# Kernel optimization log

Measured on AMD Instinct MI355X. Metric: run time of the kernel, lower is better.

## Reference

```python
import jax, jax.numpy as jnp
import numpy as np
from jax import lax

B, K, C = 8, 65536, 128
NUM_PROPOSAL = 1024


def furthest_point_sample(xyz, n):
    """xyz: (B,K,3) -> (B,n) int32 indices, matching pointnet2 FPS."""
    b, k, _ = xyz.shape
    init_far = jnp.zeros((b,), dtype=jnp.int32)          # first picked point = index 0
    init_dist = jnp.full((b, k), 1e10, dtype=xyz.dtype)  # running min squared distance

    def step(carry, _):
        dist, far = carry
        pt = jnp.take_along_axis(xyz, far[:, None, None].astype(jnp.int32), axis=1)  # (B,1,3)
        d = jnp.sum((xyz - pt) ** 2, axis=-1)            # (B,K)
        dist = jnp.minimum(dist, d)
        far = jnp.argmax(dist, axis=-1).astype(jnp.int32)
        return (dist, far), far

    (_, _), rest = lax.scan(step, (init_dist, init_far), None, length=n - 1)  # rest: (n-1,B)
    inds = jnp.concatenate([init_far[None, :], rest], axis=0)                  # (n,B)
    return jnp.transpose(inds, (1, 0))                                         # (B,n)


def setup_inputs() -> dict:
    key = jax.random.key(0)
    k1, k2 = jax.random.split(key)
    xyz = jax.random.normal(k1, (B, K, 3), dtype=jnp.float32)
    features = jax.random.normal(k2, (B, C, K), dtype=jnp.float32)
    return {"xyz": xyz, "features": features}


def reference(xyz, features):
    sample_inds = furthest_point_sample(xyz, NUM_PROPOSAL)            # (B,n)
    # gather_operation(xyz^T, inds)^T -> (B,n,3)
    new_xyz = jnp.take_along_axis(xyz, sample_inds[:, :, None], axis=1)
    # gather_operation(features, inds) -> (B,C,n)
    new_features = jnp.take_along_axis(features, sample_inds[:, None, :], axis=2)
    return (new_xyz, new_features, sample_inds)
```

## Files before the change

kernel.cpp:

```cpp
#include <hip/hip_runtime.h>
#include <stdint.h>

#define BATCH 8
#define K 65536
#define CFEAT 128
#define NPROP 1024
#define M 16
#define T 320
#define CTHREADS 256
#define PTS (K / M)
#define PPT (PTS / CTHREADS)

#define OUT_FEAT (BATCH * NPROP * 3)
#define OUT_INDS (BATCH * NPROP * 3 + BATCH * CFEAT * NPROP)

#define SLOT_STRIDE 8
#define WS_ULLS (2 * BATCH * M * SLOT_STRIDE)

__global__ __launch_bounds__(256) void fps_init(unsigned long long* ws) {
    int i = blockIdx.x * 256 + threadIdx.x;
    if (i < WS_ULLS) ws[i] = 0ull;
}

__device__ __forceinline__ unsigned int wave_umax63(unsigned int x) {
    int v = (int)x;
    int t;
    t = __builtin_amdgcn_update_dpp(v, v, 0x111, 0xF, 0xF, false);
    v = ((unsigned)t > (unsigned)v) ? t : v;
    t = __builtin_amdgcn_update_dpp(v, v, 0x112, 0xF, 0xF, false);
    v = ((unsigned)t > (unsigned)v) ? t : v;
    t = __builtin_amdgcn_update_dpp(v, v, 0x114, 0xF, 0xF, false);
    v = ((unsigned)t > (unsigned)v) ? t : v;
    t = __builtin_amdgcn_update_dpp(v, v, 0x118, 0xF, 0xF, false);
    v = ((unsigned)t > (unsigned)v) ? t : v;
    t = __builtin_amdgcn_update_dpp(v, v, 0x142, 0xF, 0xF, false);
    v = ((unsigned)t > (unsigned)v) ? t : v;
    t = __builtin_amdgcn_update_dpp(v, v, 0x143, 0xF, 0xF, false);
    v = ((unsigned)t > (unsigned)v) ? t : v;
    return (unsigned int)v;
}

__device__ __forceinline__ unsigned int row16_umax15(unsigned int x) {
    int v = (int)x;
    int t;
    t = __builtin_amdgcn_update_dpp(v, v, 0x111, 0xF, 0xF, false);
    v = ((unsigned)t > (unsigned)v) ? t : v;
    t = __builtin_amdgcn_update_dpp(v, v, 0x112, 0xF, 0xF, false);
    v = ((unsigned)t > (unsigned)v) ? t : v;
    t = __builtin_amdgcn_update_dpp(v, v, 0x114, 0xF, 0xF, false);
    v = ((unsigned)t > (unsigned)v) ? t : v;
    t = __builtin_amdgcn_update_dpp(v, v, 0x118, 0xF, 0xF, false);
    v = ((unsigned)t > (unsigned)v) ? t : v;
    return (unsigned int)v;
}

__global__ __launch_bounds__(T) void fps_kernel(const float* __restrict__ xyz,
                                                float* __restrict__ out,
                                                unsigned long long* __restrict__ ws) {
    const int b = blockIdx.x & 7;
    const int w = blockIdx.x >> 3;
    const int tid = threadIdx.x;
    const int lane = tid & 63;
    const int wv = tid >> 6;
    const float* xb = xyz + (size_t)b * (K * 3);
    const int base = w * PTS;

    __shared__ unsigned long long s_wkey[4];
    __shared__ unsigned int s_res;

    float px[PPT], py[PPT], pz[PPT], dist[PPT];
    if (wv < 4) {
#pragma unroll
        for (int j = 0; j < PPT; ++j) {
            int l = j * CTHREADS + tid;
            int g = base + l;
            px[j] = xb[3 * g];
            py[j] = xb[3 * g + 1];
            pz[j] = xb[3 * g + 2];
            dist[j] = 1e10f;
        }
    }
    float qx = xb[0], qy = xb[1], qz = xb[2];
    if (tid == 0) {
        s_wkey[0] = 0ull; s_wkey[1] = 0ull; s_wkey[2] = 0ull; s_wkey[3] = 0ull;
        s_res = 0u;
        if (w == 0) out[OUT_INDS + b * NPROP] = 0.0f;
    }
    __syncthreads();

    if (wv < 4) {
        for (int t = 1; t < NPROP; ++t) {
            float bestd = -1.0f;
            unsigned int bestl = 0;
#pragma unroll
            for (int j = 0; j < PPT; ++j) {
                float dx = __fsub_rn(px[j], qx);
                float dy = __fsub_rn(py[j], qy);
                float dz = __fsub_rn(pz[j], qz);
                float d = __fadd_rn(__fadd_rn(__fmul_rn(dx, dx), __fmul_rn(dy, dy)),
                                    __fmul_rn(dz, dz));
                float nd = fminf(dist[j], d);
                dist[j] = nd;
                unsigned int l = (unsigned int)(j * CTHREADS + tid);
                bool gt = nd > bestd;
                bestd = gt ? nd : bestd;
                bestl = gt ? l : bestl;
            }
            unsigned int du = __float_as_uint(bestd);
            unsigned int m1 = wave_umax63(du);
            unsigned int maxd = (unsigned int)__builtin_amdgcn_readlane((int)m1, 63);
            unsigned int cand = (du == maxd) ? ~bestl : 0u;
            unsigned int m2 = wave_umax63(cand);
            if (lane == 63) {
                unsigned int l = ~m2;
                unsigned int g = (unsigned int)base + l;
                unsigned long long key =
                    ((unsigned long long)maxd << 32) |
                    ((unsigned long long)((0xFFFFu - g) & 0xFFFFu) << 16) |
                    (unsigned long long)(unsigned int)t;
                __hip_atomic_store(&s_wkey[wv], key, __ATOMIC_RELAXED,
                                   __HIP_MEMORY_SCOPE_WORKGROUP);
            }
            unsigned int r;
            do {
                r = __hip_atomic_load(&s_res, __ATOMIC_RELAXED,
                                      __HIP_MEMORY_SCOPE_WORKGROUP);
            } while ((r & 0xFFFFu) != (unsigned int)t);
            unsigned int g = r >> 16;
            qx = xb[3 * g];
            qy = xb[3 * g + 1];
            qz = xb[3 * g + 2];
        }
    } else {
        for (int t = 1; t < NPROP; ++t) {
            const int par = t & 1;
            unsigned long long* sgrp =
                ws + (size_t)((par * BATCH + b) * M) * SLOT_STRIDE;
            const unsigned int tt = (unsigned int)t;
            if (lane < M) {
                unsigned long long kk;
                do {
                    kk = __hip_atomic_load(&s_wkey[lane & 3], __ATOMIC_RELAXED,
                                           __HIP_MEMORY_SCOPE_WORKGROUP);
                } while ((kk & 0xFFFFu) != (unsigned long long)tt);
                unsigned int hi = (unsigned int)(kk >> 32);
                unsigned int lo = (unsigned int)kk;
                unsigned int p1 = row16_umax15(hi);
                unsigned int mh = (unsigned int)__builtin_amdgcn_readlane((int)p1, 15);
                unsigned int c2 = (hi == mh) ? lo : 0u;
                unsigned int p2 = row16_umax15(c2);
                unsigned int ml = (unsigned int)__builtin_amdgcn_readlane((int)p2, 15);
                if (lane == 0) {
                    unsigned long long kb = ((unsigned long long)mh << 32) |
                                            (unsigned long long)ml;
                    __hip_atomic_store(&sgrp[(size_t)w * SLOT_STRIDE], kb,
                                       __ATOMIC_RELAXED, __HIP_MEMORY_SCOPE_AGENT);
                }
                unsigned int khi, klo;
                if (lane == w) {
                    khi = mh; klo = ml;
                } else {
                    unsigned long long* sp = sgrp + (size_t)lane * SLOT_STRIDE;
                    unsigned long long v;
                    do {
                        v = __hip_atomic_load(sp, __ATOMIC_RELAXED,
                                              __HIP_MEMORY_SCOPE_AGENT);
                    } while ((unsigned short)v != (unsigned short)tt);
                    khi = (unsigned int)(v >> 32);
                    klo = (unsigned int)v;
                }
                unsigned int q1 = row16_umax15(khi);
                unsigned int qh = (unsigned int)__builtin_amdgcn_readlane((int)q1, 15);
                unsigned int d2 = (khi == qh) ? klo : 0u;
                unsigned int q2 = row16_umax15(d2);
                unsigned int ql = (unsigned int)__builtin_amdgcn_readlane((int)q2, 15);
                unsigned int g = 0xFFFFu - (ql >> 16);
                if (lane == 0) {
                    __hip_atomic_store(&s_res, (g << 16) | tt, __ATOMIC_RELAXED,
                                       __HIP_MEMORY_SCOPE_WORKGROUP);
                    if (w == 0) out[OUT_INDS + b * NPROP + t] = (float)g;
                }
            }
        }
    }
}

__global__ __launch_bounds__(256) void gather_kernel(const float* __restrict__ xyz,
                                                     const float* __restrict__ feat,
                                                     float* __restrict__ out) {
    int gid = blockIdx.x * 256 + threadIdx.x;
    int n = gid & (NPROP - 1);
    int b = gid >> 17;
    int c = (gid >> 10) & (CFEAT - 1);
    int ind = (int)out[OUT_INDS + (b << 10) + n];
    out[OUT_FEAT + gid] = feat[(((size_t)b * CFEAT + c) << 16) + (size_t)ind];
    if (gid < BATCH * NPROP) {
        int b2 = gid >> 10;
        int ind2 = (int)out[OUT_INDS + gid];
        const float* s = xyz + ((size_t)b2 * K + (size_t)ind2) * 3;
        float a0 = s[0], a1 = s[1], a2 = s[2];
        out[gid * 3 + 0] = a0;
        out[gid * 3 + 1] = a1;
        out[gid * 3 + 2] = a2;
    }
}

extern "C" void kernel_launch(void* const* d_in, const int* in_sizes, int n_in,
                              void* d_out, int out_size, void* d_ws, size_t ws_size,
                              hipStream_t stream) {
    const float* xyz = (const float*)d_in[0];
    const float* feat = (const float*)d_in[1];
    float* out = (float*)d_out;
    unsigned long long* ws = (unsigned long long*)d_ws;

    hipLaunchKernelGGL(fps_init, dim3(WS_ULLS / 256), dim3(256), 0, stream, ws);
    hipLaunchKernelGGL(fps_kernel, dim3(BATCH * M), dim3(T), 0, stream,
                       xyz, out, ws);
    hipLaunchKernelGGL(gather_kernel, dim3(BATCH * CFEAT * NPROP / 256), dim3(256),
                       0, stream, xyz, feat, out);
}
```

Before: 2.021 ms.

## Publish per-wave keys directly to global slots, reduce across all 64 in one wave

Each compute wave now writes its candidate key straight to a global slot (64 slots per batch, one per wave across the 16 blocks). The coordinator wave no longer runs a two-level reduction (block reduce, publish, then cross-block reduce). Instead, after waiting on the local shared keys and a short sleep, it polls all 64 global slots and does a single 64-lane DPP reduction. This removes one serial hop of global publish and poll latency on the per-iteration critical path, at the cost of more global atomic traffic and polling per step.

```diff
diff --git a/kernel.cpp b/kernel.cpp
--- a/kernel.cpp
+++ b/kernel.cpp
@@ -10,12 +10,13 @@
 #define CTHREADS 256
 #define PTS (K / M)
 #define PPT (PTS / CTHREADS)
+#define NSLOT 64
 
 #define OUT_FEAT (BATCH * NPROP * 3)
 #define OUT_INDS (BATCH * NPROP * 3 + BATCH * CFEAT * NPROP)
 
 #define SLOT_STRIDE 8
-#define WS_ULLS (2 * BATCH * M * SLOT_STRIDE)
+#define WS_ULLS (2 * BATCH * NSLOT * SLOT_STRIDE)
 
 __global__ __launch_bounds__(256) void fps_init(unsigned long long* ws) {
     int i = blockIdx.x * 256 + threadIdx.x;
@@ -40,20 +41,6 @@
     return (unsigned int)v;
 }
 
-__device__ __forceinline__ unsigned int row16_umax15(unsigned int x) {
-    int v = (int)x;
-    int t;
-    t = __builtin_amdgcn_update_dpp(v, v, 0x111, 0xF, 0xF, false);
-    v = ((unsigned)t > (unsigned)v) ? t : v;
-    t = __builtin_amdgcn_update_dpp(v, v, 0x112, 0xF, 0xF, false);
-    v = ((unsigned)t > (unsigned)v) ? t : v;
-    t = __builtin_amdgcn_update_dpp(v, v, 0x114, 0xF, 0xF, false);
-    v = ((unsigned)t > (unsigned)v) ? t : v;
-    t = __builtin_amdgcn_update_dpp(v, v, 0x118, 0xF, 0xF, false);
-    v = ((unsigned)t > (unsigned)v) ? t : v;
-    return (unsigned int)v;
-}
-
 __global__ __launch_bounds__(T) void fps_kernel(const float* __restrict__ xyz,
                                                 float* __restrict__ out,
                                                 unsigned long long* __restrict__ ws) {
@@ -68,8 +55,15 @@
     __shared__ unsigned long long s_wkey[4];
     __shared__ unsigned int s_res;
 
-    float px[PPT], py[PPT], pz[PPT], dist[PPT];
+    if (tid == 0) {
+        s_wkey[0] = 0ull; s_wkey[1] = 0ull; s_wkey[2] = 0ull; s_wkey[3] = 0ull;
+        s_res = 0u;
+        if (w == 0) out[OUT_INDS + b * NPROP] = 0.0f;
+    }
+    __syncthreads();
+
     if (wv < 4) {
+        float px[PPT], py[PPT], pz[PPT], dist[PPT];
 #pragma unroll
         for (int j = 0; j < PPT; ++j) {
             int l = j * CTHREADS + tid;
@@ -79,16 +73,8 @@
             pz[j] = xb[3 * g + 2];
             dist[j] = 1e10f;
         }
-    }
-    float qx = xb[0], qy = xb[1], qz = xb[2];
-    if (tid == 0) {
-        s_wkey[0] = 0ull; s_wkey[1] = 0ull; s_wkey[2] = 0ull; s_wkey[3] = 0ull;
-        s_res = 0u;
-        if (w == 0) out[OUT_INDS + b * NPROP] = 0.0f;
-    }
-    __syncthreads();
+        float qx = xb[0], qy = xb[1], qz = xb[2];
 
-    if (wv < 4) {
         for (int t = 1; t < NPROP; ++t) {
             float bestd = -1.0f;
             unsigned int bestl = 0;
@@ -118,6 +104,10 @@
                     ((unsigned long long)maxd << 32) |
                     ((unsigned long long)((0xFFFFu - g) & 0xFFFFu) << 16) |
                     (unsigned long long)(unsigned int)t;
+                __hip_atomic_store(
+                    &ws[((size_t)(((t & 1) * BATCH + b) * NSLOT) +
+                         (size_t)(w * 4 + wv)) * SLOT_STRIDE],
+                    key, __ATOMIC_RELAXED, __HIP_MEMORY_SCOPE_AGENT);
                 __hip_atomic_store(&s_wkey[wv], key, __ATOMIC_RELAXED,
                                    __HIP_MEMORY_SCOPE_WORKGROUP);
             }
@@ -133,53 +123,35 @@
         }
     } else {
         for (int t = 1; t < NPROP; ++t) {
-            const int par = t & 1;
+            const unsigned int tt = (unsigned int)t;
             unsigned long long* sgrp =
-                ws + (size_t)((par * BATCH + b) * M) * SLOT_STRIDE;
-            const unsigned int tt = (unsigned int)t;
-            if (lane < M) {
+                ws + (size_t)(((t & 1) * BATCH + b) * NSLOT) * SLOT_STRIDE;
+            if (lane < 4) {
                 unsigned long long kk;
                 do {
-                    kk = __hip_atomic_load(&s_wkey[lane & 3], __ATOMIC_RELAXED,
+                    kk = __hip_atomic_load(&s_wkey[lane], __ATOMIC_RELAXED,
                                            __HIP_MEMORY_SCOPE_WORKGROUP);
                 } while ((kk & 0xFFFFu) != (unsigned long long)tt);
-                unsigned int hi = (unsigned int)(kk >> 32);
-                unsigned int lo = (unsigned int)kk;
-                unsigned int p1 = row16_umax15(hi);
-                unsigned int mh = (unsigned int)__builtin_amdgcn_readlane((int)p1, 15);
-                unsigned int c2 = (hi == mh) ? lo : 0u;
-                unsigned int p2 = row16_umax15(c2);
-                unsigned int ml = (unsigned int)__builtin_amdgcn_readlane((int)p2, 15);
-                if (lane == 0) {
-                    unsigned long long kb = ((unsigned long long)mh << 32) |
-                                            (unsigned long long)ml;
-                    __hip_atomic_store(&sgrp[(size_t)w * SLOT_STRIDE], kb,
-                                       __ATOMIC_RELAXED, __HIP_MEMORY_SCOPE_AGENT);
-                }
-                unsigned int khi, klo;
-                if (lane == w) {
-                    khi = mh; klo = ml;
-                } else {
-                    unsigned long long* sp = sgrp + (size_t)lane * SLOT_STRIDE;
-                    unsigned long long v;
-                    do {
-                        v = __hip_atomic_load(sp, __ATOMIC_RELAXED,
-                                              __HIP_MEMORY_SCOPE_AGENT);
-                    } while ((unsigned short)v != (unsigned short)tt);
-                    khi = (unsigned int)(v >> 32);
-                    klo = (unsigned int)v;
-                }
-                unsigned int q1 = row16_umax15(khi);
-                unsigned int qh = (unsigned int)__builtin_amdgcn_readlane((int)q1, 15);
-                unsigned int d2 = (khi == qh) ? klo : 0u;
-                unsigned int q2 = row16_umax15(d2);
-                unsigned int ql = (unsigned int)__builtin_amdgcn_readlane((int)q2, 15);
-                unsigned int g = 0xFFFFu - (ql >> 16);
-                if (lane == 0) {
-                    __hip_atomic_store(&s_res, (g << 16) | tt, __ATOMIC_RELAXED,
-                                       __HIP_MEMORY_SCOPE_WORKGROUP);
-                    if (w == 0) out[OUT_INDS + b * NPROP + t] = (float)g;
-                }
+            }
+            __builtin_amdgcn_s_sleep(6);
+            unsigned long long* sp = sgrp + (size_t)lane * SLOT_STRIDE;
+            unsigned long long v;
+            do {
+                v = __hip_atomic_load(sp, __ATOMIC_RELAXED,
+                                      __HIP_MEMORY_SCOPE_AGENT);
+            } while ((unsigned short)v != (unsigned short)tt);
+            unsigned int hi = (unsigned int)(v >> 32);
+            unsigned int lo = (unsigned int)v;
+            unsigned int p1 = wave_umax63(hi);
+            unsigned int mh = (unsigned int)__builtin_amdgcn_readlane((int)p1, 63);
+            unsigned int c2 = (hi == mh) ? lo : 0u;
+            unsigned int p2 = wave_umax63(c2);
+            unsigned int ml = (unsigned int)__builtin_amdgcn_readlane((int)p2, 63);
+            unsigned int g = 0xFFFFu - (ml >> 16);
+            if (lane == 0) {
+                __hip_atomic_store(&s_res, (g << 16) | tt, __ATOMIC_RELAXED,
+                                   __HIP_MEMORY_SCOPE_WORKGROUP);
+                if (w == 0) out[OUT_INDS + b * NPROP + t] = (float)g;
             }
         }
     }
```

Result: faster. 1.735 ms (-14.2%).
